# Kernel tuning notes

Measured on AMD Instinct MI355X. Metric: run time of the kernel, lower is better.

Reference implementation:

```python
import jax, jax.numpy as jnp
import numpy as np

N, M, E, F, OUT = 20000, 2048, 320000, 512, 2
HID = F // 2
NEG_ATT = 0.2   # leaky_relu slope inside HypergraphConv attention
NEG = 0.01      # default F.leaky_relu / nn.LeakyReLU slope
EPS = 1e-5      # GraphNorm eps


def setup_inputs() -> dict:
    key = jax.random.key(0)
    ks = jax.random.split(key, 12)
    nrm = lambda k, shape, s=0.05: (jax.random.normal(k, shape, jnp.float32) * s)
    row = jax.random.randint(ks[1], (E,), 0, N)
    col = jax.random.randint(ks[2], (E,), 0, M)
    return dict(
        x=nrm(ks[0], (N, F), 1.0),
        edge_index=jnp.stack([row, col]),                 # [2, E] int32
        edge_attr=nrm(ks[3], (M, F), 1.0),
        W1=nrm(ks[4], (F, F)), att1=nrm(ks[5], (2 * F,)), b1=jnp.zeros((F,), jnp.float32),
        W2=nrm(ks[6], (F, F)), att2=nrm(ks[7], (2 * F,)), b2=jnp.zeros((F,), jnp.float32),
        gn1_w=jnp.ones((F,), jnp.float32), gn1_b=jnp.zeros((F,), jnp.float32), gn1_ms=jnp.ones((F,), jnp.float32),
        gn2_w=jnp.ones((F,), jnp.float32), gn2_b=jnp.zeros((F,), jnp.float32), gn2_ms=jnp.ones((F,), jnp.float32),
        fc1_W=nrm(ks[8], (F, HID)), fc1_b=jnp.zeros((HID,), jnp.float32),
        fc2_W=nrm(ks[9], (F, HID)), fc2_b=jnp.zeros((HID,), jnp.float32),
        cls_W=nrm(ks[10], (HID, OUT)), cls_b=jnp.zeros((OUT,), jnp.float32),
    )


def _segsum(v, idx, n):
    return jax.ops.segment_sum(v, idx, num_segments=n)


def hypergraph_conv(x, edge_attr, row, col, W, att, bias):
    """PyG HypergraphConv, heads=1, use_attention=True, attention_mode='node'."""
    xl = x @ W                          # [N, F] node features after lin
    el = edge_attr @ W                  # [M, F] hyperedge features after lin
    # attention logits per incidence: (cat[x_i, e_j] * att).sum(-1)
    pre = xl[row] @ att[:F] + el[col] @ att[F:]           # [E]
    alpha = jax.nn.leaky_relu(pre, NEG_ATT)
    # softmax grouped by hyperedge (col)
    amax = jax.ops.segment_max(alpha, col, num_segments=M)
    amax = jnp.where(jnp.isfinite(amax), amax, 0.0)
    ex = jnp.exp(alpha - amax[col])
    denom = _segsum(ex, col, M)
    alpha = ex / jnp.maximum(denom, 1e-16)[col]           # [E]
    # degree normalizations (hyperedge_weight = 1)
    ones = jnp.ones((row.shape[0],), xl.dtype)
    deg_n = _segsum(ones, row, N)
    Dinv = jnp.where(deg_n > 0, 1.0 / deg_n, 0.0)         # [N]
    deg_e = _segsum(ones, col, M)
    Binv = jnp.where(deg_e > 0, 1.0 / deg_e, 0.0)         # [M]
    # propagate 1: nodes -> hyperedges
    edge_feat = _segsum((alpha * Binv[col])[:, None] * xl[row], col, M)   # [M, F]
    # propagate 2: hyperedges -> nodes
    out = _segsum((alpha * Dinv[row])[:, None] * edge_feat[col], row, N)  # [N, F]
    return out + bias


def graph_norm(x, w, b, ms):
    # single graph (batch=None): normalize over all nodes
    mean = x.mean(axis=0)
    out = x - ms * mean
    var = (out * out).mean(axis=0)
    return out / jnp.sqrt(var + EPS) * w + b


def reference(x, edge_index, edge_attr,
              W1, att1, b1, W2, att2, b2,
              gn1_w, gn1_b, gn1_ms, gn2_w, gn2_b, gn2_ms,
              fc1_W, fc1_b, fc2_W, fc2_b, cls_W, cls_b):
    row, col = edge_index[0], edge_index[1]
    h = hypergraph_conv(x, edge_attr, row, col, W1, att1, b1)
    h = jax.nn.leaky_relu(graph_norm(h, gn1_w, gn1_b, gn1_ms), NEG)
    out = jax.nn.leaky_relu(h @ fc1_W + fc1_b, NEG)
    h = hypergraph_conv(h, edge_attr, row, col, W2, att2, b2)
    h = jax.nn.leaky_relu(graph_norm(h, gn2_w, gn2_b, gn2_ms), NEG)
    out = out + jax.nn.leaky_relu(h @ fc2_W + fc2_b, NEG)
    logits = out @ cls_W + cls_b
    return logits
```

## Files before the change

### kernel.cpp

```cpp
#include <hip/hip_runtime.h>
#include <math.h>

#define FDIM 512
#define HIDDIM 256
#define HB 128
#define SCH 1024
#define LDSK 32

typedef __bf16 bf16x8 __attribute__((ext_vector_type(8)));
typedef float floatx4 __attribute__((ext_vector_type(4)));

__device__ __forceinline__ float lrelu(float x, float s) { return x >= 0.0f ? x : s * x; }

__device__ __forceinline__ float bf2f(unsigned int u) {
  union { float f; unsigned int i; } v; v.i = u << 16; return v.f;
}
__device__ __forceinline__ unsigned short f2bf(float f) {
  union { float f; unsigned int u; } v; v.f = f;
  unsigned int x = v.u;
  return (unsigned short)((x + 0x7fffu + ((x >> 16) & 1u)) >> 16);
}

__device__ __forceinline__ void async_copy16(const unsigned short* g, unsigned short* l) {
  __builtin_amdgcn_global_load_lds((const __attribute__((address_space(1))) unsigned int*)g,
                                   (__attribute__((address_space(3))) unsigned int*)l, 16, 0, 0);
}

__device__ __forceinline__ float waveReduceSum(float v) {
#pragma unroll
  for (int o = 32; o; o >>= 1) v += __shfl_down(v, o, 64);
  return v;
}

__device__ __forceinline__ float blockReduceSum256(float v) {
  __shared__ float sm[4];
  int lane = threadIdx.x & 63, w = threadIdx.x >> 6;
  v = waveReduceSum(v);
  __syncthreads();
  if (lane == 0) sm[w] = v;
  __syncthreads();
  return sm[0] + sm[1] + sm[2] + sm[3];
}

__device__ __forceinline__ float blockReduceMax256(float v) {
  __shared__ float sm[4];
  int lane = threadIdx.x & 63, w = threadIdx.x >> 6;
#pragma unroll
  for (int o = 32; o; o >>= 1) v = fmaxf(v, __shfl_down(v, o, 64));
  __syncthreads();
  if (lane == 0) sm[w] = v;
  __syncthreads();
  return fmaxf(fmaxf(sm[0], sm[1]), fmaxf(sm[2], sm[3]));
}

__global__ __launch_bounds__(256) void k_hist2(const int* __restrict__ row, const int* __restrict__ col,
                                               int* __restrict__ cnt_r, int* __restrict__ cnt_c,
                                               int E, int nchunk) {
  __shared__ int h[2048];
  int b = blockIdx.x, t = threadIdx.x;
  for (int i = t; i < 2048; i += 256) h[i] = 0;
  __syncthreads();
  int s = b * nchunk, e = min(E, s + nchunk);
  for (int j = s + t; j < e; j += 256) {
    atomicAdd(&h[col[j]], 1);
    atomicAdd(&cnt_r[row[j]], 1);
  }
  __syncthreads();
  for (int i = t; i < 2048; i += 256) {
    int v = h[i];
    if (v) atomicAdd(&cnt_c[i], v);
  }
}

__global__ __launch_bounds__(256) void k_scan_part(const int* __restrict__ cnt, int* __restrict__ off,
                                                   int* __restrict__ btot, int n) {
  int b = blockIdx.x, t = threadIdx.x;
  int base = b * SCH + t * 4;
  int v[4];
#pragma unroll
  for (int i = 0; i < 4; ++i) v[i] = (base + i < n) ? cnt[base + i] : 0;
  int s = v[0] + v[1] + v[2] + v[3];
  int lane = t & 63, w = t >> 6;
  int x = s;
#pragma unroll
  for (int o = 1; o < 64; o <<= 1) {
    int y = __shfl_up(x, o, 64);
    if (lane >= o) x += y;
  }
  __shared__ int ws[4];
  if (lane == 63) ws[w] = x;
  __syncthreads();
  int wpre = 0;
  for (int i = 0; i < w; ++i) wpre += ws[i];
  int run = wpre + x - s;
#pragma unroll
  for (int i = 0; i < 4; ++i) {
    if (base + i < n) off[base + i] = run;
    run += v[i];
  }
  if (t == 255) btot[b] = wpre + x;
}

__global__ __launch_bounds__(256) void k_scan_mid(int* __restrict__ btot, int nb) {
  int t = threadIdx.x;
  int v = (t < nb) ? btot[t] : 0;
  int lane = t & 63, w = t >> 6;
  int x = v;
#pragma unroll
  for (int o = 1; o < 64; o <<= 1) {
    int y = __shfl_up(x, o, 64);
    if (lane >= o) x += y;
  }
  __shared__ int ws[4];
  if (lane == 63) ws[w] = x;
  __syncthreads();
  int wpre = 0;
  for (int i = 0; i < w; ++i) wpre += ws[i];
  if (t < nb) btot[t] = wpre + x - v;
  if (t == 255) btot[nb] = wpre + x;
}

__global__ __launch_bounds__(256) void k_scan_add(int* __restrict__ off, const int* __restrict__ btot,
                                                  int n, int nb) {
  int b = blockIdx.x, t = threadIdx.x;
  int base = b * SCH + t * 4;
  int add = btot[b];
#pragma unroll
  for (int i = 0; i < 4; ++i)
    if (base + i < n) off[base + i] += add;
  if (b == 0 && t == 0) off[n] = btot[nb];
}

__global__ __launch_bounds__(256) void k_scan2048(const int* __restrict__ cnt, int* __restrict__ off,
                                                  int* __restrict__ gcur) {
  int t = threadIdx.x;
  int base = t * 8;
  int v[8];
#pragma unroll
  for (int i = 0; i < 8; ++i) v[i] = cnt[base + i];
  int s = 0;
#pragma unroll
  for (int i = 0; i < 8; ++i) s += v[i];
  int lane = t & 63, w = t >> 6;
  int x = s;
#pragma unroll
  for (int o = 1; o < 64; o <<= 1) {
    int y = __shfl_up(x, o, 64);
    if (lane >= o) x += y;
  }
  __shared__ int ws[4];
  if (lane == 63) ws[w] = x;
  __syncthreads();
  int wpre = 0;
  for (int i = 0; i < w; ++i) wpre += ws[i];
  int run = wpre + x - s;
#pragma unroll
  for (int i = 0; i < 8; ++i) {
    off[base + i] = run;
    gcur[base + i] = run;
    run += v[i];
  }
  if (t == 255) off[2048] = wpre + x;
}

__global__ __launch_bounds__(256) void k_fill3(const int* __restrict__ row, const int* __restrict__ col,
                                               int* __restrict__ gcur, const int* __restrict__ off_r,
                                               int* __restrict__ cur_r, int* __restrict__ csr_c,
                                               int* __restrict__ rj, int* __restrict__ cj,
                                               int* __restrict__ pos_r, int E, int nchunk) {
  __shared__ int h[2048];
  __shared__ int lbase[2048];
  int b = blockIdx.x, t = threadIdx.x;
  for (int i = t; i < 2048; i += 256) h[i] = 0;
  __syncthreads();
  int s = b * nchunk, e = min(E, s + nchunk);
  for (int j = s + t; j < e; j += 256) atomicAdd(&h[col[j]], 1);
  __syncthreads();
  for (int i = t; i < 2048; i += 256) {
    int c = h[i];
    lbase[i] = c ? atomicAdd(&gcur[i], c) : 0;
    h[i] = 0;
  }
  __syncthreads();
  for (int j = s + t; j < e; j += 256) {
    int r = row[j], c = col[j];
    int slot_c = lbase[c] + atomicAdd(&h[c], 1);
    csr_c[slot_c] = j;
    rj[slot_c] = r;
    int slot_r = off_r[r] + atomicAdd(&cur_r[r], 1);
    cj[slot_r] = c;
    pos_r[j] = slot_r;
  }
}

__global__ __launch_bounds__(256) void k_hi(const float* __restrict__ A, unsigned short* __restrict__ hi, int n4) {
  int i = blockIdx.x * 256 + threadIdx.x;
  if (i < n4) {
    float4 v = ((const float4*)A)[i];
    ushort4 h;
    h.x = f2bf(v.x); h.y = f2bf(v.y); h.z = f2bf(v.z); h.w = f2bf(v.w);
    ((ushort4*)hi)[i] = h;
  }
}

__global__ __launch_bounds__(256) void k_prep_w_hi(const float* __restrict__ W, unsigned short* __restrict__ th,
                                                   int K, int Nc) {
  int n = blockIdx.x * 16 + (threadIdx.x & 15);
  int k = blockIdx.y * 16 + (threadIdx.x >> 4);
  th[(size_t)n * K + k] = f2bf(W[(size_t)k * Nc + n]);
}

__global__ __launch_bounds__(256) void k_prep_w(const float* __restrict__ W, unsigned short* __restrict__ th,
                                                unsigned short* __restrict__ tl, int K, int Nc) {
  int n = blockIdx.x * 16 + (threadIdx.x & 15);
  int k = blockIdx.y * 16 + (threadIdx.x >> 4);
  float v = W[(size_t)k * Nc + n];
  unsigned short h = f2bf(v);
  unsigned short l = f2bf(v - bf2f(h));
  th[(size_t)n * K + k] = h;
  tl[(size_t)n * K + k] = l;
}

__global__ __launch_bounds__(256) void k_wv(const float* __restrict__ W, const float* __restrict__ att,
                                            float* __restrict__ wv) {
  int lane = threadIdx.x & 63, w = threadIdx.x >> 6;
  int k = blockIdx.x * 4 + w;
  float s = 0.f;
  for (int f = lane; f < FDIM; f += 64) s = fmaf(W[(size_t)k * FDIM + f], att[f], s);
  s = waveReduceSum(s);
  if (lane == 0) wv[k] = s;
}

__global__ __launch_bounds__(256) void k_ea(const float* __restrict__ X, const float* __restrict__ wv,
                                            float* __restrict__ out, int Mr) {
  int lane = threadIdx.x & 63, w = threadIdx.x >> 6;
  int m = blockIdx.x * 4 + w;
  if (m < Mr) {
    float s = 0.f;
    for (int f = lane; f < FDIM; f += 64) s = fmaf(X[(size_t)m * FDIM + f], wv[f], s);
    s = waveReduceSum(s);
    if (lane == 0) out[m] = s;
  }
}

__global__ __launch_bounds__(256, 1) void gemm_conv(const unsigned short* __restrict__ Ah,
                                                    const unsigned short* __restrict__ Bth,
                                                    unsigned short* __restrict__ Cb,
                                                    const float* __restrict__ att, float* __restrict__ xa,
                                                    int Mr, int K, int Nc) {
  __shared__ unsigned short lds[2 * 128 * LDSK];
  int tid = threadIdx.x, lane = tid & 63, w = tid >> 6;
  int wr = w >> 1, wc = w & 1;
  int rowB = blockIdx.x * 128, colB = blockIdx.y * 128;

  const unsigned short* src = (w < 2) ? Ah : Bth;
  int baseRow = ((w < 2) ? rowB : colB) + 64 * (w & 1);
  int maxRow = (w < 2) ? (Mr - 1) : (Nc - 1);
  int slr = lane >> 2, slc = lane & 3;
  unsigned short* dstBase = &lds[((w >> 1) * 128 + (w & 1) * 64) * LDSK];

  size_t gro[4];
#pragma unroll
  for (int seg = 0; seg < 4; ++seg) {
    int rg = baseRow + seg * 16 + slr;
    if (rg > maxRow) rg = maxRow;
    gro[seg] = (size_t)rg * K + slc * 8;
  }

  floatx4 zero4 = {0.f, 0.f, 0.f, 0.f};
  floatx4 acc[4][4];
#pragma unroll
  for (int i = 0; i < 4; ++i)
#pragma unroll
    for (int j = 0; j < 4; ++j) acc[i][j] = zero4;

  int fr = lane & 15, fq = lane >> 4;
  int offA = (wr * 64 + fr) * LDSK + fq * 8;
  int offB = 128 * LDSK + (wc * 64 + fr) * LDSK + fq * 8;

  for (int k0 = 0; k0 < K; k0 += 32) {
#pragma unroll
    for (int seg = 0; seg < 4; ++seg) async_copy16(src + gro[seg] + k0, dstBase + seg * 16 * LDSK);
    __syncthreads();
    bf16x8 a[4], b[4];
#pragma unroll
    for (int t = 0; t < 4; ++t) {
      a[t] = *(const bf16x8*)(&lds[offA + t * 16 * LDSK]);
      b[t] = *(const bf16x8*)(&lds[offB + t * 16 * LDSK]);
    }
#pragma unroll
    for (int ti = 0; ti < 4; ++ti)
#pragma unroll
      for (int tj = 0; tj < 4; ++tj)
        acc[ti][tj] = __builtin_amdgcn_mfma_f32_16x16x32_bf16(a[ti], b[tj], acc[ti][tj], 0, 0, 0);
    __syncthreads();
  }

  int colL = colB + wc * 64 + fr;
  int rowL = rowB + wr * 64 + fq * 4;
  float attv[4];
#pragma unroll
  for (int tj = 0; tj < 4; ++tj) attv[tj] = att[colL + tj * 16];
#pragma unroll
  for (int ti = 0; ti < 4; ++ti) {
#pragma unroll
    for (int r = 0; r < 4; ++r) {
      int rr = rowL + ti * 16 + r;
      if (rr < Mr) {
        float dot = 0.f;
#pragma unroll
        for (int tj = 0; tj < 4; ++tj) {
          float v = acc[ti][tj][r];
          Cb[(size_t)rr * Nc + colL + tj * 16] = f2bf(v);
          dot = fmaf(v, attv[tj], dot);
        }
#pragma unroll
        for (int o = 1; o < 16; o <<= 1) dot += __shfl_xor(dot, o, 64);
        if ((lane & 15) == 0) atomicAdd(&xa[rr], dot);
      }
    }
  }
}

template <int EPI>
__global__ __launch_bounds__(256, 1) void gemm_fc(const unsigned short* __restrict__ Ahi,
                                                  const unsigned short* __restrict__ Alo,
                                                  const unsigned short* __restrict__ Bthi,
                                                  const unsigned short* __restrict__ Btlo,
                                                  float* __restrict__ Cf, const float* __restrict__ bias,
                                                  int Mr, int K, int Nc) {
  __shared__ unsigned short lds[(2 * 128 + 2 * 64) * LDSK];
  int tid = threadIdx.x, lane = tid & 63, w = tid >> 6;
  int wr = w >> 1, wc = w & 1;
  int rowB = blockIdx.x * 128, colB = blockIdx.y * 64;

  const unsigned short* src = (w == 0) ? Ahi : (w == 1) ? Alo : (w == 2) ? Bthi : Btlo;
  int baseRow = (w < 2) ? rowB : colB;
  int maxRow = (w < 2) ? (Mr - 1) : (Nc - 1);
  int nseg = (w < 2) ? 8 : 4;
  int slr = lane >> 2, slc = lane & 3;
  unsigned short* dstBase = &lds[((w < 2) ? (w * 128) : (256 + (w - 2) * 64)) * LDSK];

  size_t gro[8];
  for (int seg = 0; seg < nseg; ++seg) {
    int rg = baseRow + seg * 16 + slr;
    if (rg > maxRow) rg = maxRow;
    gro[seg] = (size_t)rg * K + slc * 8;
  }

  floatx4 zero4 = {0.f, 0.f, 0.f, 0.f};
  floatx4 acc[4][2];
#pragma unroll
  for (int i = 0; i < 4; ++i) {
    acc[i][0] = zero4;
    acc[i][1] = zero4;
  }

  int fr = lane & 15, fq = lane >> 4;
  int offA = (wr * 64 + fr) * LDSK + fq * 8;
  int offB = 256 * LDSK + (wc * 32 + fr) * LDSK + fq * 8;

  for (int k0 = 0; k0 < K; k0 += 32) {
    for (int seg = 0; seg < nseg; ++seg) async_copy16(src + gro[seg] + k0, dstBase + seg * 16 * LDSK);
    __syncthreads();
    bf16x8 ah[4], al[4], bh[2], bl[2];
#pragma unroll
    for (int t = 0; t < 4; ++t) {
      ah[t] = *(const bf16x8*)(&lds[offA + t * 16 * LDSK]);
      al[t] = *(const bf16x8*)(&lds[128 * LDSK + offA + t * 16 * LDSK]);
    }
#pragma unroll
    for (int t = 0; t < 2; ++t) {
      bh[t] = *(const bf16x8*)(&lds[offB + t * 16 * LDSK]);
      bl[t] = *(const bf16x8*)(&lds[64 * LDSK + offB + t * 16 * LDSK]);
    }
#pragma unroll
    for (int ti = 0; ti < 4; ++ti)
#pragma unroll
      for (int tj = 0; tj < 2; ++tj) {
        acc[ti][tj] = __builtin_amdgcn_mfma_f32_16x16x32_bf16(ah[ti], bh[tj], acc[ti][tj], 0, 0, 0);
        acc[ti][tj] = __builtin_amdgcn_mfma_f32_16x16x32_bf16(ah[ti], bl[tj], acc[ti][tj], 0, 0, 0);
        acc[ti][tj] = __builtin_amdgcn_mfma_f32_16x16x32_bf16(al[ti], bh[tj], acc[ti][tj], 0, 0, 0);
      }
    __syncthreads();
  }

  int colL = colB + wc * 32 + fr;
  int rowL = rowB + wr * 64 + fq * 4;
#pragma unroll
  for (int tj = 0; tj < 2; ++tj) {
    int c = colL + tj * 16;
    float bb = bias[c];
#pragma unroll
    for (int ti = 0; ti < 4; ++ti) {
#pragma unroll
      for (int r = 0; r < 4; ++r) {
        int rr = rowL + ti * 16 + r;
        if (rr < Mr) {
          float v = lrelu(acc[ti][tj][r] + bb, 0.01f);
          if (EPI == 1) Cf[(size_t)rr * Nc + c] = v;
          else Cf[(size_t)rr * Nc + c] += v;
        }
      }
    }
  }
}

__global__ __launch_bounds__(256) void k_attn(const float* __restrict__ xa, const float* __restrict__ ea,
                                              const int* __restrict__ rj, const int* __restrict__ csr_c,
                                              const int* __restrict__ pos_r, const int* __restrict__ off_c,
                                              float* __restrict__ aj, float* __restrict__ arj) {
  int m = blockIdx.x;
  int s = off_c[m], e_ = off_c[m + 1];
  float eam = ea[m];
  int t = threadIdx.x;
  float mx = -3.402823466e38f;
  for (int j = s + t; j < e_; j += 256) {
    float a = lrelu(xa[rj[j]] + eam, 0.2f);
    aj[j] = a;
    mx = fmaxf(mx, a);
  }
  mx = blockReduceMax256(mx);
  float sum = 0.f;
  for (int j = s + t; j < e_; j += 256) sum += expf(aj[j] - mx);
  sum = blockReduceSum256(sum);
  float inv = 1.0f / fmaxf(sum, 1e-16f);
  for (int j = s + t; j < e_; j += 256) {
    float a = expf(aj[j] - mx) * inv;
    aj[j] = a;
    arj[pos_r[csr_c[j]]] = a;
  }
}

__global__ __launch_bounds__(256) void k_prop_col(const unsigned short* __restrict__ xl,
                                                  const float* __restrict__ aj, const int* __restrict__ rj,
                                                  const int* __restrict__ off_c, unsigned short* __restrict__ ef) {
  int m = blockIdx.x;
  int s = off_c[m], e_ = off_c[m + 1];
  int cnt = e_ - s;
  __shared__ int sidx[512];
  __shared__ float swgt[512];
  __shared__ float pf[4][512];
  int t = threadIdx.x, lane = t & 63, w = t >> 6;
  float acc[8] = {0, 0, 0, 0, 0, 0, 0, 0};
  for (int base = 0; base < cnt; base += 512) {
    int n = min(512, cnt - base);
    for (int j = t; j < n; j += 256) {
      sidx[j] = rj[s + base + j];
      swgt[j] = aj[s + base + j];
    }
    __syncthreads();
    int j = w;
    for (; j + 8 <= n; j += 8) {
      int r0 = sidx[j], r1 = sidx[j + 4];
      float w0 = swgt[j], w1 = swgt[j + 4];
      bf16x8 v0 = *(const bf16x8*)(xl + (size_t)r0 * FDIM + lane * 8);
      bf16x8 v1 = *(const bf16x8*)(xl + (size_t)r1 * FDIM + lane * 8);
#pragma unroll
      for (int i = 0; i < 8; ++i) acc[i] = fmaf(w0, (float)v0[i], acc[i]);
#pragma unroll
      for (int i = 0; i < 8; ++i) acc[i] = fmaf(w1, (float)v1[i], acc[i]);
    }
    for (; j < n; j += 4) {
      int r = sidx[j];
      float wt = swgt[j];
      bf16x8 v = *(const bf16x8*)(xl + (size_t)r * FDIM + lane * 8);
#pragma unroll
      for (int i = 0; i < 8; ++i) acc[i] = fmaf(wt, (float)v[i], acc[i]);
    }
    __syncthreads();
  }
  float binv = cnt > 0 ? 1.0f / (float)cnt : 0.0f;
#pragma unroll
  for (int i = 0; i < 8; i += 2) *(float2*)&pf[w][lane * 8 + i] = make_float2(acc[i] * binv, acc[i + 1] * binv);
  __syncthreads();
  float2 r0 = ((const float2*)pf[0])[t], r1 = ((const float2*)pf[1])[t];
  float2 r2 = ((const float2*)pf[2])[t], r3 = ((const float2*)pf[3])[t];
  float a0 = r0.x + r1.x + r2.x + r3.x;
  float a1 = r0.y + r1.y + r2.y + r3.y;
  unsigned int o = (unsigned int)f2bf(a0) | ((unsigned int)f2bf(a1) << 16);
  ((unsigned int*)(ef + (size_t)m * FDIM))[t] = o;
}

__global__ __launch_bounds__(256) void k_prop_row(const unsigned short* __restrict__ ef,
                                                  const float* __restrict__ arj, const int* __restrict__ cj,
                                                  const int* __restrict__ off_r, const float* __restrict__ bias,
                                                  unsigned short* __restrict__ hb) {
  int nB = blockIdx.x;
  int s = off_r[nB], e_ = off_r[nB + 1];
  int cnt = e_ - s;
  __shared__ int sidx[512];
  __shared__ float swgt[512];
  __shared__ float pf[4][512];
  int t = threadIdx.x, lane = t & 63, w = t >> 6;
  float acc[8] = {0, 0, 0, 0, 0, 0, 0, 0};
  for (int base = 0; base < cnt; base += 512) {
    int n = min(512, cnt - base);
    for (int j = t; j < n; j += 256) {
      sidx[j] = cj[s + base + j];
      swgt[j] = arj[s + base + j];
    }
    __syncthreads();
    int j = w;
    for (; j + 8 <= n; j += 8) {
      int r0 = sidx[j], r1 = sidx[j + 4];
      float w0 = swgt[j], w1 = swgt[j + 4];
      bf16x8 v0 = *(const bf16x8*)(ef + (size_t)r0 * FDIM + lane * 8);
      bf16x8 v1 = *(const bf16x8*)(ef + (size_t)r1 * FDIM + lane * 8);
#pragma unroll
      for (int i = 0; i < 8; ++i) acc[i] = fmaf(w0, (float)v0[i], acc[i]);
#pragma unroll
      for (int i = 0; i < 8; ++i) acc[i] = fmaf(w1, (float)v1[i], acc[i]);
    }
    for (; j < n; j += 4) {
      int r = sidx[j];
      float wt = swgt[j];
      bf16x8 v = *(const bf16x8*)(ef + (size_t)r * FDIM + lane * 8);
#pragma unroll
      for (int i = 0; i < 8; ++i) acc[i] = fmaf(wt, (float)v[i], acc[i]);
    }
    __syncthreads();
  }
  float dinv = cnt > 0 ? 1.0f / (float)cnt : 0.0f;
#pragma unroll
  for (int i = 0; i < 8; i += 2) *(float2*)&pf[w][lane * 8 + i] = make_float2(acc[i] * dinv, acc[i + 1] * dinv);
  __syncthreads();
  float2 r0 = ((const float2*)pf[0])[t], r1 = ((const float2*)pf[1])[t];
  float2 r2 = ((const float2*)pf[2])[t], r3 = ((const float2*)pf[3])[t];
  float a0 = r0.x + r1.x + r2.x + r3.x + bias[2 * t];
  float a1 = r0.y + r1.y + r2.y + r3.y + bias[2 * t + 1];
  unsigned int o = (unsigned int)f2bf(a0) | ((unsigned int)f2bf(a1) << 16);
  ((unsigned int*)(hb + (size_t)nB * FDIM))[t] = o;
}

__global__ __launch_bounds__(256) void k_stats(const unsigned short* __restrict__ hb, float* __restrict__ gsum,
                                               float* __restrict__ gsq, int N) {
  int t = threadIdx.x;
  float s0 = 0, q0 = 0, s1 = 0, q1 = 0;
  for (int r = blockIdx.x; r < N; r += gridDim.x) {
    unsigned int u = ((const unsigned int*)(hb + (size_t)r * FDIM))[t];
    float v0 = bf2f(u & 0xffffu), v1 = bf2f(u >> 16);
    s0 += v0; q0 = fmaf(v0, v0, q0);
    s1 += v1; q1 = fmaf(v1, v1, q1);
  }
  atomicAdd(&gsum[2 * t], s0);
  atomicAdd(&gsq[2 * t], q0);
  atomicAdd(&gsum[2 * t + 1], s1);
  atomicAdd(&gsq[2 * t + 1], q1);
}

__global__ __launch_bounds__(512) void k_nparam(const float* __restrict__ gsum, const float* __restrict__ gsq,
                                                const float* __restrict__ ms, const float* __restrict__ w,
                                                float* __restrict__ msm, float* __restrict__ scl, float invn) {
  int f = threadIdx.x;
  float mean = gsum[f] * invn;
  float ex2 = gsq[f] * invn;
  float m = ms[f];
  float var = ex2 - (2.0f * m - m * m) * mean * mean;
  scl[f] = w[f] / sqrtf(var + 1e-5f);
  msm[f] = m * mean;
}

__global__ __launch_bounds__(256) void k_napply(const unsigned short* __restrict__ hb,
                                                const float* __restrict__ msm, const float* __restrict__ scl,
                                                const float* __restrict__ b, unsigned short* __restrict__ hi,
                                                unsigned short* __restrict__ lo, int total2) {
  int i = blockIdx.x * 256 + threadIdx.x;
  if (i < total2) {
    int f2 = i & 255;
    unsigned int u = ((const unsigned int*)hb)[i];
    float v0 = bf2f(u & 0xffffu), v1 = bf2f(u >> 16);
    int f0 = 2 * f2, f1 = 2 * f2 + 1;
    v0 = lrelu((v0 - msm[f0]) * scl[f0] + b[f0], 0.01f);
    v1 = lrelu((v1 - msm[f1]) * scl[f1] + b[f1], 0.01f);
    unsigned short h0 = f2bf(v0), h1 = f2bf(v1);
    unsigned short l0 = f2bf(v0 - bf2f(h0)), l1 = f2bf(v1 - bf2f(h1));
    ((unsigned int*)hi)[i] = (unsigned int)h0 | ((unsigned int)h1 << 16);
    ((unsigned int*)lo)[i] = (unsigned int)l0 | ((unsigned int)l1 << 16);
  }
}

__global__ __launch_bounds__(256) void k_cls(const float* __restrict__ out1, const float* __restrict__ W,
                                             const float* __restrict__ b, float* __restrict__ logits, int N) {
  __shared__ float Ws[512];
  int t = threadIdx.x;
  Ws[t] = W[t];
  Ws[256 + t] = W[256 + t];
  __syncthreads();
  int lane = t & 63, w = t >> 6;
  int r = blockIdx.x * 4 + w;
  if (r < N) {
    float a0 = 0.f, a1 = 0.f;
    for (int k = lane; k < 256; k += 64) {
      float v = out1[(size_t)r * 256 + k];
      a0 = fmaf(v, Ws[2 * k], a0);
      a1 = fmaf(v, Ws[2 * k + 1], a1);
    }
#pragma unroll
    for (int o = 32; o; o >>= 1) {
      a0 += __shfl_down(a0, o, 64);
      a1 += __shfl_down(a1, o, 64);
    }
    if (lane == 0) {
      logits[(size_t)r * 2] = a0 + b[0];
      logits[(size_t)r * 2 + 1] = a1 + b[1];
    }
  }
}

extern "C" void kernel_launch(void* const* d_in, const int* in_sizes, int n_in,
                              void* d_out, int out_size, void* d_ws, size_t ws_size,
                              hipStream_t stream) {
  const float* x      = (const float*)d_in[0];
  const int*   eidx   = (const int*)d_in[1];
  const float* eattr  = (const float*)d_in[2];
  const float* W1     = (const float*)d_in[3];
  const float* att1   = (const float*)d_in[4];
  const float* b1     = (const float*)d_in[5];
  const float* W2     = (const float*)d_in[6];
  const float* att2   = (const float*)d_in[7];
  const float* b2     = (const float*)d_in[8];
  const float* gn1_w  = (const float*)d_in[9];
  const float* gn1_b  = (const float*)d_in[10];
  const float* gn1_ms = (const float*)d_in[11];
  const float* gn2_w  = (const float*)d_in[12];
  const float* gn2_b  = (const float*)d_in[13];
  const float* gn2_ms = (const float*)d_in[14];
  const float* fc1_W  = (const float*)d_in[15];
  const float* fc1_b  = (const float*)d_in[16];
  const float* fc2_W  = (const float*)d_in[17];
  const float* fc2_b  = (const float*)d_in[18];
  const float* cls_W  = (const float*)d_in[19];
  const float* cls_b  = (const float*)d_in[20];
  float* logits = (float*)d_out;

  const int N = in_sizes[0] / FDIM;
  const int E = in_sizes[1] / 2;
  const int M = in_sizes[2] / FDIM;
  const int* row = eidx;
  const int* col = eidx + E;
  const size_t NS = (size_t)N * FDIM;
  const size_t MS = (size_t)M * FDIM;

  char* base = (char*)d_ws;
  auto alloc = [&](size_t bytes) { char* r = base; base += (bytes + 255) & ~(size_t)255; return r; };

  unsigned short* xhi = (unsigned short*)alloc(NS * 2);
  unsigned short* xlo = (unsigned short*)alloc(NS * 2);
  unsigned short* xl  = (unsigned short*)alloc(NS * 2);
  unsigned short* hb  = (unsigned short*)alloc(NS * 2);
  unsigned short* ef  = (unsigned short*)alloc(MS * 2);
  float* out1 = (float*)alloc((size_t)N * HIDDIM * 4);
  unsigned short* w1th = (unsigned short*)alloc(FDIM * FDIM * 2);
  unsigned short* w2th = (unsigned short*)alloc(FDIM * FDIM * 2);
  unsigned short* f1th = (unsigned short*)alloc(FDIM * HIDDIM * 2);
  unsigned short* f1tl = (unsigned short*)alloc(FDIM * HIDDIM * 2);
  unsigned short* f2th = (unsigned short*)alloc(FDIM * HIDDIM * 2);
  unsigned short* f2tl = (unsigned short*)alloc(FDIM * HIDDIM * 2);
  float* wv1 = (float*)alloc(FDIM * 4);
  float* wv2 = (float*)alloc(FDIM * 4);
  float* xa = (float*)alloc((size_t)N * 4);
  float* ea1 = (float*)alloc((size_t)M * 4);
  float* ea2 = (float*)alloc((size_t)M * 4);
  float* aj  = (float*)alloc((size_t)E * 4);
  float* arj = (float*)alloc((size_t)E * 4);
  float* gsum = (float*)alloc(FDIM * 4);
  float* gsq  = (float*)alloc(FDIM * 4);
  float* msm  = (float*)alloc(FDIM * 4);
  float* scl  = (float*)alloc(FDIM * 4);
  int* cnt_r = (int*)alloc((size_t)(2 * N + M) * 4);
  int* cur_r = cnt_r + N;
  int* cnt_c = cur_r + N;
  int* off_r = (int*)alloc((size_t)(N + 1) * 4);
  int* off_c = (int*)alloc((size_t)(M + 1) * 4);
  int* gcur  = (int*)alloc((size_t)M * 4);
  int* csr_c = (int*)alloc((size_t)E * 4);
  int* rj    = (int*)alloc((size_t)E * 4);
  int* cj    = (int*)alloc((size_t)E * 4);
  int* pos_r = (int*)alloc((size_t)E * 4);
  int* btot  = (int*)alloc(512 * 4);

  hipMemsetAsync(cnt_r, 0, sizeof(int) * (size_t)(2 * N + M), stream);

  int nchunk = (E + HB - 1) / HB;
  int nbR = (N + SCH - 1) / SCH;
  k_hist2<<<HB, 256, 0, stream>>>(row, col, cnt_r, cnt_c, E, nchunk);
  k_scan_part<<<nbR, 256, 0, stream>>>(cnt_r, off_r, btot, N);
  k_scan_mid<<<1, 256, 0, stream>>>(btot, nbR);
  k_scan_add<<<nbR, 256, 0, stream>>>(off_r, btot, N, nbR);
  k_scan2048<<<1, 256, 0, stream>>>(cnt_c, off_c, gcur);
  k_fill3<<<HB, 256, 0, stream>>>(row, col, gcur, off_r, cur_r, csr_c, rj, cj, pos_r, E, nchunk);

  k_hi<<<(int)((NS / 4 + 255) / 256), 256, 0, stream>>>(x, xhi, (int)(NS / 4));
  k_prep_w_hi<<<dim3(FDIM / 16, FDIM / 16), 256, 0, stream>>>(W1, w1th, FDIM, FDIM);
  k_prep_w_hi<<<dim3(FDIM / 16, FDIM / 16), 256, 0, stream>>>(W2, w2th, FDIM, FDIM);
  k_prep_w<<<dim3(HIDDIM / 16, FDIM / 16), 256, 0, stream>>>(fc1_W, f1th, f1tl, FDIM, HIDDIM);
  k_prep_w<<<dim3(HIDDIM / 16, FDIM / 16), 256, 0, stream>>>(fc2_W, f2th, f2tl, FDIM, HIDDIM);
  k_wv<<<FDIM / 4, 256, 0, stream>>>(W1, att1 + FDIM, wv1);
  k_wv<<<FDIM / 4, 256, 0, stream>>>(W2, att2 + FDIM, wv2);
  k_ea<<<(M + 3) / 4, 256, 0, stream>>>(eattr, wv1, ea1, M);
  k_ea<<<(M + 3) / 4, 256, 0, stream>>>(eattr, wv2, ea2, M);

  int gN128 = (N + 127) / 128;
  int napply_grid = (int)((NS / 2 + 255) / 256);

  hipMemsetAsync(xa, 0, (size_t)N * 4, stream);
  gemm_conv<<<dim3(gN128, FDIM / 128), 256, 0, stream>>>(xhi, w1th, xl, att1, xa, N, FDIM, FDIM);
  k_attn<<<M, 256, 0, stream>>>(xa, ea1, rj, csr_c, pos_r, off_c, aj, arj);
  k_prop_col<<<M, 256, 0, stream>>>(xl, aj, rj, off_c, ef);
  k_prop_row<<<N, 256, 0, stream>>>(ef, arj, cj, off_r, b1, hb);
  hipMemsetAsync(gsum, 0, sizeof(float) * 2 * FDIM, stream);
  k_stats<<<256, 256, 0, stream>>>(hb, gsum, gsq, N);
  k_nparam<<<1, 512, 0, stream>>>(gsum, gsq, gn1_ms, gn1_w, msm, scl, 1.0f / (float)N);
  k_napply<<<napply_grid, 256, 0, stream>>>(hb, msm, scl, gn1_b, xhi, xlo, (int)(NS / 2));
  gemm_fc<1><<<dim3(gN128, HIDDIM / 64), 256, 0, stream>>>(xhi, xlo, f1th, f1tl, out1, fc1_b, N, FDIM, HIDDIM);

  hipMemsetAsync(xa, 0, (size_t)N * 4, stream);
  gemm_conv<<<dim3(gN128, FDIM / 128), 256, 0, stream>>>(xhi, w2th, xl, att2, xa, N, FDIM, FDIM);
  k_attn<<<M, 256, 0, stream>>>(xa, ea2, rj, csr_c, pos_r, off_c, aj, arj);
  k_prop_col<<<M, 256, 0, stream>>>(xl, aj, rj, off_c, ef);
  k_prop_row<<<N, 256, 0, stream>>>(ef, arj, cj, off_r, b2, hb);
  hipMemsetAsync(gsum, 0, sizeof(float) * 2 * FDIM, stream);
  k_stats<<<256, 256, 0, stream>>>(hb, gsum, gsq, N);
  k_nparam<<<1, 512, 0, stream>>>(gsum, gsq, gn2_ms, gn2_w, msm, scl, 1.0f / (float)N);
  k_napply<<<napply_grid, 256, 0, stream>>>(hb, msm, scl, gn2_b, xhi, xlo, (int)(NS / 2));
  gemm_fc<2><<<dim3(gN128, HIDDIM / 64), 256, 0, stream>>>(xhi, xlo, f2th, f2tl, out1, fc2_b, N, FDIM, HIDDIM);

  k_cls<<<(N + 3) / 4, 256, 0, stream>>>(out1, cls_W, cls_b, logits, N);
}
```

Before: 605.6 us.

## Drop bf16 lo split for activations in fc GEMMs, widen tile, swap grid axes

```diff
diff --git a/kernel.cpp b/kernel.cpp
--- a/kernel.cpp
+++ b/kernel.cpp
@@ -251,7 +251,7 @@
   __shared__ unsigned short lds[2 * 128 * LDSK];
   int tid = threadIdx.x, lane = tid & 63, w = tid >> 6;
   int wr = w >> 1, wc = w & 1;
-  int rowB = blockIdx.x * 128, colB = blockIdx.y * 128;
+  int rowB = blockIdx.y * 128, colB = blockIdx.x * 128;
 
   const unsigned short* src = (w < 2) ? Ah : Bth;
   int baseRow = ((w < 2) ? rowB : colB) + 64 * (w & 1);
@@ -324,23 +324,23 @@
 
 template <int EPI>
 __global__ __launch_bounds__(256, 1) void gemm_fc(const unsigned short* __restrict__ Ahi,
-                                                  const unsigned short* __restrict__ Alo,
                                                   const unsigned short* __restrict__ Bthi,
                                                   const unsigned short* __restrict__ Btlo,
                                                   float* __restrict__ Cf, const float* __restrict__ bias,
                                                   int Mr, int K, int Nc) {
-  __shared__ unsigned short lds[(2 * 128 + 2 * 64) * LDSK];
+  __shared__ unsigned short lds[3 * 128 * LDSK];
   int tid = threadIdx.x, lane = tid & 63, w = tid >> 6;
   int wr = w >> 1, wc = w & 1;
-  int rowB = blockIdx.x * 128, colB = blockIdx.y * 64;
-
-  const unsigned short* src = (w == 0) ? Ahi : (w == 1) ? Alo : (w == 2) ? Bthi : Btlo;
-  int baseRow = (w < 2) ? rowB : colB;
-  int maxRow = (w < 2) ? (Mr - 1) : (Nc - 1);
-  int nseg = (w < 2) ? 8 : 4;
+  int rowB = blockIdx.y * 128, colB = blockIdx.x * 128;
+
+  const unsigned short* src;
+  int baseRow, maxRow, nseg;
+  unsigned short* dstBase;
+  if (w < 2) { src = Ahi; baseRow = rowB + 64 * w; maxRow = Mr - 1; nseg = 4; dstBase = &lds[w * 64 * LDSK]; }
+  else if (w == 2) { src = Bthi; baseRow = colB; maxRow = Nc - 1; nseg = 8; dstBase = &lds[128 * LDSK]; }
+  else { src = Btlo; baseRow = colB; maxRow = Nc - 1; nseg = 8; dstBase = &lds[2 * 128 * LDSK]; }
+
   int slr = lane >> 2, slc = lane & 3;
-  unsigned short* dstBase = &lds[((w < 2) ? (w * 128) : (256 + (w - 2) * 64)) * LDSK];
-
   size_t gro[8];
   for (int seg = 0; seg < nseg; ++seg) {
     int rg = baseRow + seg * 16 + slr;
@@ -349,46 +349,40 @@
   }
 
   floatx4 zero4 = {0.f, 0.f, 0.f, 0.f};
-  floatx4 acc[4][2];
-#pragma unroll
-  for (int i = 0; i < 4; ++i) {
-    acc[i][0] = zero4;
-    acc[i][1] = zero4;
-  }
+  floatx4 acc[4][4];
+#pragma unroll
+  for (int i = 0; i < 4; ++i)
+#pragma unroll
+    for (int j = 0; j < 4; ++j) acc[i][j] = zero4;
 
   int fr = lane & 15, fq = lane >> 4;
   int offA = (wr * 64 + fr) * LDSK + fq * 8;
-  int offB = 256 * LDSK + (wc * 32 + fr) * LDSK + fq * 8;
+  int offBh = 128 * LDSK + (wc * 64 + fr) * LDSK + fq * 8;
 
   for (int k0 = 0; k0 < K; k0 += 32) {
     for (int seg = 0; seg < nseg; ++seg) async_copy16(src + gro[seg] + k0, dstBase + seg * 16 * LDSK);
     __syncthreads();
-    bf16x8 ah[4], al[4], bh[2], bl[2];
+    bf16x8 a[4], bh[4], bl[4];
 #pragma unroll
     for (int t = 0; t < 4; ++t) {
-      ah[t] = *(const bf16x8*)(&lds[offA + t * 16 * LDSK]);
-      al[t] = *(const bf16x8*)(&lds[128 * LDSK + offA + t * 16 * LDSK]);
-    }
-#pragma unroll
-    for (int t = 0; t < 2; ++t) {
-      bh[t] = *(const bf16x8*)(&lds[offB + t * 16 * LDSK]);
-      bl[t] = *(const bf16x8*)(&lds[64 * LDSK + offB + t * 16 * LDSK]);
+      a[t] = *(const bf16x8*)(&lds[offA + t * 16 * LDSK]);
+      bh[t] = *(const bf16x8*)(&lds[offBh + t * 16 * LDSK]);
+      bl[t] = *(const bf16x8*)(&lds[128 * LDSK + offBh + t * 16 * LDSK]);
     }
 #pragma unroll
     for (int ti = 0; ti < 4; ++ti)
 #pragma unroll
-      for (int tj = 0; tj < 2; ++tj) {
-        acc[ti][tj] = __builtin_amdgcn_mfma_f32_16x16x32_bf16(ah[ti], bh[tj], acc[ti][tj], 0, 0, 0);
-        acc[ti][tj] = __builtin_amdgcn_mfma_f32_16x16x32_bf16(ah[ti], bl[tj], acc[ti][tj], 0, 0, 0);
-        acc[ti][tj] = __builtin_amdgcn_mfma_f32_16x16x32_bf16(al[ti], bh[tj], acc[ti][tj], 0, 0, 0);
+      for (int tj = 0; tj < 4; ++tj) {
+        acc[ti][tj] = __builtin_amdgcn_mfma_f32_16x16x32_bf16(a[ti], bh[tj], acc[ti][tj], 0, 0, 0);
+        acc[ti][tj] = __builtin_amdgcn_mfma_f32_16x16x32_bf16(a[ti], bl[tj], acc[ti][tj], 0, 0, 0);
       }
     __syncthreads();
   }
 
-  int colL = colB + wc * 32 + fr;
+  int colL = colB + wc * 64 + fr;
   int rowL = rowB + wr * 64 + fq * 4;
 #pragma unroll
-  for (int tj = 0; tj < 2; ++tj) {
+  for (int tj = 0; tj < 4; ++tj) {
     int c = colL + tj * 16;
     float bb = bias[c];
 #pragma unroll
@@ -564,7 +558,7 @@
 __global__ __launch_bounds__(256) void k_napply(const unsigned short* __restrict__ hb,
                                                 const float* __restrict__ msm, const float* __restrict__ scl,
                                                 const float* __restrict__ b, unsigned short* __restrict__ hi,
-                                                unsigned short* __restrict__ lo, int total2) {
+                                                int total2) {
   int i = blockIdx.x * 256 + threadIdx.x;
   if (i < total2) {
     int f2 = i & 255;
@@ -573,10 +567,7 @@
     int f0 = 2 * f2, f1 = 2 * f2 + 1;
     v0 = lrelu((v0 - msm[f0]) * scl[f0] + b[f0], 0.01f);
     v1 = lrelu((v1 - msm[f1]) * scl[f1] + b[f1], 0.01f);
-    unsigned short h0 = f2bf(v0), h1 = f2bf(v1);
-    unsigned short l0 = f2bf(v0 - bf2f(h0)), l1 = f2bf(v1 - bf2f(h1));
-    ((unsigned int*)hi)[i] = (unsigned int)h0 | ((unsigned int)h1 << 16);
-    ((unsigned int*)lo)[i] = (unsigned int)l0 | ((unsigned int)l1 << 16);
+    ((unsigned int*)hi)[i] = (unsigned int)f2bf(v0) | ((unsigned int)f2bf(v1) << 16);
   }
 }
 
@@ -646,7 +637,6 @@
   auto alloc = [&](size_t bytes) { char* r = base; base += (bytes + 255) & ~(size_t)255; return r; };
 
   unsigned short* xhi = (unsigned short*)alloc(NS * 2);
-  unsigned short* xlo = (unsigned short*)alloc(NS * 2);
   unsigned short* xl  = (unsigned short*)alloc(NS * 2);
   unsigned short* hb  = (unsigned short*)alloc(NS * 2);
   unsigned short* ef  = (unsigned short*)alloc(MS * 2);
@@ -705,26 +695,26 @@
   int napply_grid = (int)((NS / 2 + 255) / 256);
 
   hipMemsetAsync(xa, 0, (size_t)N * 4, stream);
-  gemm_conv<<<dim3(gN128, FDIM / 128), 256, 0, stream>>>(xhi, w1th, xl, att1, xa, N, FDIM, FDIM);
+  gemm_conv<<<dim3(FDIM / 128, gN128), 256, 0, stream>>>(xhi, w1th, xl, att1, xa, N, FDIM, FDIM);
   k_attn<<<M, 256, 0, stream>>>(xa, ea1, rj, csr_c, pos_r, off_c, aj, arj);
   k_prop_col<<<M, 256, 0, stream>>>(xl, aj, rj, off_c, ef);
   k_prop_row<<<N, 256, 0, stream>>>(ef, arj, cj, off_r, b1, hb);
   hipMemsetAsync(gsum, 0, sizeof(float) * 2 * FDIM, stream);
   k_stats<<<256, 256, 0, stream>>>(hb, gsum, gsq, N);
   k_nparam<<<1, 512, 0, stream>>>(gsum, gsq, gn1_ms, gn1_w, msm, scl, 1.0f / (float)N);
-  k_napply<<<napply_grid, 256, 0, stream>>>(hb, msm, scl, gn1_b, xhi, xlo, (int)(NS / 2));
-  gemm_fc<1><<<dim3(gN128, HIDDIM / 64), 256, 0, stream>>>(xhi, xlo, f1th, f1tl, out1, fc1_b, N, FDIM, HIDDIM);
+  k_napply<<<napply_grid, 256, 0, stream>>>(hb, msm, scl, gn1_b, xhi, (int)(NS / 2));
+  gemm_fc<1><<<dim3(HIDDIM / 128, gN128), 256, 0, stream>>>(xhi, f1th, f1tl, out1, fc1_b, N, FDIM, HIDDIM);
 
   hipMemsetAsync(xa, 0, (size_t)N * 4, stream);
-  gemm_conv<<<dim3(gN128, FDIM / 128), 256, 0, stream>>>(xhi, w2th, xl, att2, xa, N, FDIM, FDIM);
+  gemm_conv<<<dim3(FDIM / 128, gN128), 256, 0, stream>>>(xhi, w2th, xl, att2, xa, N, FDIM, FDIM);
   k_attn<<<M, 256, 0, stream>>>(xa, ea2, rj, csr_c, pos_r, off_c, aj, arj);
   k_prop_col<<<M, 256, 0, stream>>>(xl, aj, rj, off_c, ef);
   k_prop_row<<<N, 256, 0, stream>>>(ef, arj, cj, off_r, b2, hb);
   hipMemsetAsync(gsum, 0, sizeof(float) * 2 * FDIM, stream);
   k_stats<<<256, 256, 0, stream>>>(hb, gsum, gsq, N);
   k_nparam<<<1, 512, 0, stream>>>(gsum, gsq, gn2_ms, gn2_w, msm, scl, 1.0f / (float)N);
-  k_napply<<<napply_grid, 256, 0, stream>>>(hb, msm, scl, gn2_b, xhi, xlo, (int)(NS / 2));
-  gemm_fc<2><<<dim3(gN128, HIDDIM / 64), 256, 0, stream>>>(xhi, xlo, f2th, f2tl, out1, fc2_b, N, FDIM, HIDDIM);
+  k_napply<<<napply_grid, 256, 0, stream>>>(hb, msm, scl, gn2_b, xhi, (int)(NS / 2));
+  gemm_fc<2><<<dim3(HIDDIM / 128, gN128), 256, 0, stream>>>(xhi, f2th, f2tl, out1, fc2_b, N, FDIM, HIDDIM);
 
   k_cls<<<(N + 3) / 4, 256, 0, stream>>>(out1, cls_W, cls_b, logits, N);
 }
```

New measurement: 598.2 us. No clear change (-1.2%).
